# Optimization experiments

Measured on AMD Instinct MI355X. Metric: run time of the kernel, lower is better.

Reference implementation:

```python
import jax, jax.numpy as jnp
import numpy as np

GLYPH_DIM = 4096
PADDING_IDX = GLYPH_DIM  # 4096
GLYPH_EMB = 20           # CHAR_EMB 16 + COLOR_EMB 4
HIDDEN = 32
MAX_LEN = 64


def setup_inputs() -> dict:
    key = jax.random.key(0)
    k1, k2, k3, k4, k5, k6, k7 = jax.random.split(key, 7)
    B, H, W = 8192, 21, 79
    glyph_chars = jax.random.randint(k1, (B, H, W), 0, 256, dtype=jnp.int32)
    glyph_colors = jax.random.randint(k2, (B, H, W), 0, 16, dtype=jnp.int32)
    # Embedding table with zero padding row (torch padding_idx semantics)
    emb_table = jax.random.normal(k3, (GLYPH_DIM + 1, GLYPH_EMB), dtype=jnp.float32) * 0.02
    emb_table = emb_table.at[PADDING_IDX].set(0.0)
    s = 1.0 / np.sqrt(HIDDEN)
    W_ih = jax.random.uniform(k4, (HIDDEN, GLYPH_EMB), minval=-s, maxval=s, dtype=jnp.float32)
    W_hh = jax.random.uniform(k5, (HIDDEN, HIDDEN), minval=-s, maxval=s, dtype=jnp.float32)
    b_ih = jax.random.uniform(k6, (HIDDEN,), minval=-s, maxval=s, dtype=jnp.float32)
    b_hh = jax.random.uniform(k7, (HIDDEN,), minval=-s, maxval=s, dtype=jnp.float32)
    return {"glyph_chars": glyph_chars, "glyph_colors": glyph_colors,
            "emb_table": emb_table, "W_ih": W_ih, "W_hh": W_hh,
            "b_ih": b_ih, "b_hh": b_hh}


def _encode_bag(glyph_chars, glyph_colors):
    """Batched sorted-unique compaction over the bounded glyph id range."""
    B = glyph_chars.shape[0]
    g_ids = ((glyph_chars << 4) + glyph_colors).reshape(B, -1)  # [B, H*W]
    # presence[b, g] = glyph g appears in sample b (batched histogram)
    bidx = jnp.broadcast_to(jnp.arange(B, dtype=g_ids.dtype)[:, None], g_ids.shape)
    presence = jnp.zeros((B, GLYPH_DIM), dtype=bool).at[bidx, g_ids].set(True)
    # compact: present ids keep their value, absent become PADDING_IDX (=4096),
    # so sorting yields ascending unique ids followed by padding.
    ids = jnp.arange(GLYPH_DIM, dtype=jnp.int32)
    keys = jnp.where(presence, ids, jnp.int32(PADDING_IDX))
    bag = jnp.sort(keys, axis=1)[:, :MAX_LEN]  # [B, MAX_LEN]
    lengths = jnp.minimum(presence.sum(axis=1), MAX_LEN)  # [B]
    return bag, lengths


def reference(glyph_chars, glyph_colors, emb_table, W_ih, W_hh, b_ih, b_hh):
    bag, lengths = _encode_bag(glyph_chars, glyph_colors)
    emb = emb_table[bag]  # [B, MAX_LEN, GLYPH_EMB]
    B = emb.shape[0]

    # packed RNN == plain RNN where hidden state freezes past each sequence length
    xs = jnp.swapaxes(emb, 0, 1)  # [T, B, E]

    def step(h, inp):
        xt, t = inp
        h_new = jnp.tanh(xt @ W_ih.T + b_ih + h @ W_hh.T + b_hh)
        h = jnp.where((t < lengths)[:, None], h_new, h)
        return h, None

    h0 = jnp.zeros((B, HIDDEN), dtype=emb.dtype)
    h, _ = jax.lax.scan(step, h0, (xs, jnp.arange(MAX_LEN)))
    return (h, emb, bag)
```

## Files before the change

### kernel.cpp

```cpp
#include <hip/hip_runtime.h>

#define HW 1659
#define PADID 4096
#define EMB 20
#define HID 32
#define MAXLEN 64

typedef float v2f __attribute__((ext_vector_type(2)));

__global__ __launch_bounds__(128) void proj_kernel(
    const float* __restrict__ emb_table, const float* __restrict__ W_ih,
    float* __restrict__ proj)
{
    const int tid = threadIdx.x;
    const int g = blockIdx.x * 4 + (tid >> 5);
    const int j = tid & 31;
    if (g > PADID) return;
    const float* er = emb_table + (size_t)g * EMB;
    const float* wr = W_ih + j * EMB;
    float s = 0.f;
#pragma unroll
    for (int k = 0; k < EMB; k++) s += wr[k] * er[k];
    proj[(size_t)g * HID + j] = s;
}

__global__ __launch_bounds__(256) void bag_emb_kernel(
    const int* __restrict__ chars, const int* __restrict__ colors,
    const float* __restrict__ emb_table,
    float* __restrict__ out_emb, float* __restrict__ out_bag)
{
    __shared__ unsigned char pres[4096];
    __shared__ int bagl[64];
    __shared__ int wsum[4];

    const int b   = blockIdx.x;
    const int tid = threadIdx.x;
    const int lane = tid & 63;
    const int wv   = tid >> 6;

    const int base = b * HW;
    const int pe = (4 - (base & 3)) & 3;
    const int nv = (HW - pe) >> 2;
    const int nt = HW - pe - (nv << 2);
    const int4* c4 = (const int4*)(chars + base + pe);
    const int4* k4 = (const int4*)(colors + base + pe);

    int4 ca = c4[tid], ka = k4[tid];
    const bool has2 = (tid + 256) < nv;
    const int i2 = has2 ? tid + 256 : tid;
    int4 cb = c4[i2], kb = k4[i2];
    int gp = -1, gt = -1;
    if (tid < pe) gp = (chars[base + tid] << 4) + colors[base + tid];
    if (tid < nt) {
        int i = base + pe + (nv << 2) + tid;
        gt = (chars[i] << 4) + colors[i];
    }

    ((uint4*)pres)[tid] = make_uint4(0u, 0u, 0u, 0u);
    if (tid < 64) bagl[tid] = PADID;
    __syncthreads();

    pres[(ca.x << 4) + ka.x] = 1;
    pres[(ca.y << 4) + ka.y] = 1;
    pres[(ca.z << 4) + ka.z] = 1;
    pres[(ca.w << 4) + ka.w] = 1;
    if (has2) {
        pres[(cb.x << 4) + kb.x] = 1;
        pres[(cb.y << 4) + kb.y] = 1;
        pres[(cb.z << 4) + kb.z] = 1;
        pres[(cb.w << 4) + kb.w] = 1;
    }
    if (gp >= 0) pres[gp] = 1;
    if (gt >= 0) pres[gt] = 1;
    __syncthreads();

    uint4 w4 = ((const uint4*)pres)[tid];
    const unsigned M = 0x01010101u;
    int cnt = __popc(w4.x & M) + __popc(w4.y & M)
            + __popc(w4.z & M) + __popc(w4.w & M);

    int pre = cnt;
#pragma unroll
    for (int d = 1; d < 64; d <<= 1) {
        int v = __shfl_up(pre, d, 64);
        if (lane >= d) pre += v;
    }
    if (lane == 63) wsum[wv] = pre;
    __syncthreads();
    int wbase = 0;
#pragma unroll
    for (int w2 = 0; w2 < 4; w2++) wbase += (w2 < wv) ? wsum[w2] : 0;
    int p = wbase + pre - cnt;

    unsigned wrd[4] = {w4.x, w4.y, w4.z, w4.w};
#pragma unroll
    for (int c = 0; c < 4; c++) {
#pragma unroll
        for (int k = 0; k < 4; k++) {
            if ((wrd[c] >> (8 * k)) & 1) {
                if (p < 64) bagl[p] = 16 * tid + 4 * c + k;
                p++;
            }
        }
    }
    __syncthreads();

    if (tid < 64) out_bag[(size_t)b * 64 + tid] = (float)bagl[tid];

    const float4* tab4 = (const float4*)emb_table;
    float4* dst4 = (float4*)(out_emb + (size_t)b * (MAXLEN * EMB));
    for (int q = tid; q < MAXLEN * 5; q += 256) {
        int t = q / 5;
        int m = q - t * 5;
        int row = bagl[t];
        dst4[q] = tab4[row * 5 + m];
    }
}

__global__ __launch_bounds__(128, 4) void rnn_kernel(
    const float* __restrict__ proj, const float* __restrict__ bagf,
    const float* __restrict__ W_hh,
    const float* __restrict__ b_ih, const float* __restrict__ b_hh,
    float* __restrict__ out_h)
{
    __shared__ float hbuf[8][32];

    const int tid  = threadIdx.x;
    const int wv   = tid >> 6;
    const int lane = tid & 63;
    const int sl   = lane >> 4;
    const int ib   = wv * 4 + sl;
    const int jj   = lane & 15;
    const int b    = blockIdx.x * 8 + ib;

    v2f w0p[16], w1p[16];
#pragma unroll
    for (int m = 0; m < 16; m++) {
        w0p[m] = (v2f){W_hh[jj * HID + 2*m], W_hh[jj * HID + 2*m + 1]};
        w1p[m] = (v2f){W_hh[(jj+16) * HID + 2*m], W_hh[(jj+16) * HID + 2*m + 1]};
    }
    const float sb0 = b_ih[jj]      + b_hh[jj];
    const float sb1 = b_ih[jj + 16] + b_hh[jj + 16];

    const float* bps = bagf + (size_t)b * 64;

    unsigned long long mm0 = __ballot(bps[jj]      < 4095.5f);
    unsigned long long mm1 = __ballot(bps[jj + 16] < 4095.5f);
    unsigned long long mm2 = __ballot(bps[jj + 32] < 4095.5f);
    unsigned long long mm3 = __ballot(bps[jj + 48] < 4095.5f);
    const int sh = sl * 16;
    const int len = __popc((unsigned)((mm0 >> sh) & 0xFFFFu))
                  + __popc((unsigned)((mm1 >> sh) & 0xFFFFu))
                  + __popc((unsigned)((mm2 >> sh) & 0xFFFFu))
                  + __popc((unsigned)((mm3 >> sh) & 0xFFFFu));

    hbuf[ib][jj]      = 0.f;
    hbuf[ib][jj + 16] = 0.f;
    asm volatile("s_waitcnt lgkmcnt(0)" ::: "memory");

    int   idxB = (int)bps[0];
    int   idxC = (int)bps[1];
    float pv0 = proj[idxB * HID + jj];
    float pv1 = proj[idxB * HID + jj + 16];

    float h0 = 0.f, h1 = 0.f;
    for (int t = 0; t < MAXLEN; t++) {
        const int t2 = (t + 2 < MAXLEN) ? (t + 2) : (MAXLEN - 1);
        const int idxD = (int)bps[t2];
        const float pv0n = proj[idxC * HID + jj];
        const float pv1n = proj[idxC * HID + jj + 16];

        const float4* hb4 = (const float4*)hbuf[ib];
        v2f a0 = (v2f){0.f, 0.f}, a1 = a0, c0 = a0, c1 = a0;
#pragma unroll
        for (int m = 0; m < 8; m += 2) {
            float4 u = hb4[m], v = hb4[m + 1];
            v2f ulo = (v2f){u.x, u.y}, uhi = (v2f){u.z, u.w};
            v2f vlo = (v2f){v.x, v.y}, vhi = (v2f){v.z, v.w};
            a0 = __builtin_elementwise_fma(w0p[2*m],     ulo, a0);
            a0 = __builtin_elementwise_fma(w0p[2*m + 1], uhi, a0);
            a1 = __builtin_elementwise_fma(w1p[2*m],     ulo, a1);
            a1 = __builtin_elementwise_fma(w1p[2*m + 1], uhi, a1);
            c0 = __builtin_elementwise_fma(w0p[2*m + 2], vlo, c0);
            c0 = __builtin_elementwise_fma(w0p[2*m + 3], vhi, c0);
            c1 = __builtin_elementwise_fma(w1p[2*m + 2], vlo, c1);
            c1 = __builtin_elementwise_fma(w1p[2*m + 3], vhi, c1);
        }
        v2f t0 = a0 + c0;
        v2f t1 = a1 + c1;
        float s0 = sb0 + pv0 + t0.x + t0.y;
        float s1 = sb1 + pv1 + t1.x + t1.y;

        float e0 = __expf(2.f * s0);
        float e1 = __expf(2.f * s1);
        float th0 = 1.f - 2.f * __builtin_amdgcn_rcpf(e0 + 1.f);
        float th1 = 1.f - 2.f * __builtin_amdgcn_rcpf(e1 + 1.f);

        h0 = (t < len) ? th0 : h0;
        h1 = (t < len) ? th1 : h1;

        hbuf[ib][jj]      = h0;
        hbuf[ib][jj + 16] = h1;
        asm volatile("s_waitcnt lgkmcnt(0)" ::: "memory");

        pv0 = pv0n; pv1 = pv1n; idxC = idxD;
    }

    out_h[(size_t)b * HID + jj]      = h0;
    out_h[(size_t)b * HID + jj + 16] = h1;
}

__global__ __launch_bounds__(128, 4) void rnn_kernel_noproj(
    const float* __restrict__ emb, const float* __restrict__ bagf,
    const float* __restrict__ W_ih, const float* __restrict__ W_hh,
    const float* __restrict__ b_ih, const float* __restrict__ b_hh,
    float* __restrict__ out_h)
{
    __shared__ float hbuf[4][32];
    const int tid = threadIdx.x;
    const int ib  = tid >> 5;
    const int j   = tid & 31;
    const int b   = blockIdx.x * 4 + ib;

    float wih[EMB];
#pragma unroll
    for (int k = 0; k < EMB; k++) wih[k] = W_ih[j * EMB + k];
    float whh[HID];
#pragma unroll
    for (int k = 0; k < HID; k++) whh[k] = W_hh[j * HID + k];
    const float sbias = b_ih[j] + b_hh[j];

    const float* bp = bagf + (size_t)b * 64;
    unsigned long long m0 = __ballot(bp[j]      < 4095.5f);
    unsigned long long m1 = __ballot(bp[32 + j] < 4095.5f);
    const int half = ib & 1;
    const int len = __popc((unsigned)(m0 >> (half * 32)))
                  + __popc((unsigned)(m1 >> (half * 32)));

    hbuf[ib][j] = 0.f;
    asm volatile("s_waitcnt lgkmcnt(0)" ::: "memory");

    float h = 0.f;
    const float* xb = emb + (size_t)b * (MAXLEN * EMB);
    for (int t = 0; t < MAXLEN; t++) {
        const float4* xp = (const float4*)(xb + t * EMB);
        float4 x0 = xp[0], x1 = xp[1], x2 = xp[2], x3 = xp[3], x4 = xp[4];
        float s = sbias;
        const float4* hb4 = (const float4*)hbuf[ib];
#pragma unroll
        for (int m = 0; m < 8; m++) {
            float4 hv = hb4[m];
            s += whh[4*m+0]*hv.x + whh[4*m+1]*hv.y
               + whh[4*m+2]*hv.z + whh[4*m+3]*hv.w;
        }
        s += wih[0]*x0.x + wih[1]*x0.y + wih[2]*x0.z + wih[3]*x0.w;
        s += wih[4]*x1.x + wih[5]*x1.y + wih[6]*x1.z + wih[7]*x1.w;
        s += wih[8]*x2.x + wih[9]*x2.y + wih[10]*x2.z + wih[11]*x2.w;
        s += wih[12]*x3.x + wih[13]*x3.y + wih[14]*x3.z + wih[15]*x3.w;
        s += wih[16]*x4.x + wih[17]*x4.y + wih[18]*x4.z + wih[19]*x4.w;
        s = fminf(fmaxf(s, -9.f), 9.f);
        float e = __expf(2.f * s);
        float th = (e - 1.f) * __builtin_amdgcn_rcpf(e + 1.f);
        h = (t < len) ? th : h;
        hbuf[ib][j] = h;
        asm volatile("s_waitcnt lgkmcnt(0)" ::: "memory");
    }
    out_h[(size_t)b * HID + j] = h;
}

extern "C" void kernel_launch(void* const* d_in, const int* in_sizes, int n_in,
                              void* d_out, int out_size, void* d_ws, size_t ws_size,
                              hipStream_t stream) {
    const int*   chars     = (const int*)d_in[0];
    const int*   colors    = (const int*)d_in[1];
    const float* emb_table = (const float*)d_in[2];
    const float* W_ih      = (const float*)d_in[3];
    const float* W_hh      = (const float*)d_in[4];
    const float* b_ih      = (const float*)d_in[5];
    const float* b_hh      = (const float*)d_in[6];

    const int B = in_sizes[0] / HW;

    float* out     = (float*)d_out;
    float* out_h   = out;
    float* out_emb = out + (size_t)B * HID;
    float* out_bag = out_emb + (size_t)B * MAXLEN * EMB;

    const size_t proj_bytes = (size_t)(PADID + 1) * HID * sizeof(float);

    bag_emb_kernel<<<B, 256, 0, stream>>>(chars, colors, emb_table, out_emb, out_bag);

    if (ws_size >= proj_bytes) {
        float* proj = (float*)d_ws;
        proj_kernel<<<(PADID + 1 + 3) / 4, 128, 0, stream>>>(emb_table, W_ih, proj);
        rnn_kernel<<<B / 8, 128, 0, stream>>>(proj, out_bag, W_hh, b_ih, b_hh, out_h);
    } else {
        rnn_kernel_noproj<<<B / 4, 128, 0, stream>>>(out_emb, out_bag, W_ih, W_hh,
                                                     b_ih, b_hh, out_h);
    }
}
```

Baseline: 185.6 us.

## Replace LDS hidden-state broadcast with DPP lane shuffles in RNN kernel

The RNN recurrence no longer writes the hidden state to shared memory and waits on lgkmcnt every step. Instead each lane holds an interleaved pair of hidden units (2*jj, 2*jj+1) and gathers the other lanes' values through a tree of DPP xor permutes within each 16-lane group. W_hh columns are permuted to match the resulting lane order, and the launch-bounds occupancy hint drops from 4 to 2 to leave room for more registers. This removes the LDS round trip from the per-step critical path, at the cost of many DPP instructions per step. It also relies on the xor mappings being correct for the row controls used.

```diff
diff --git a/kernel.cpp b/kernel.cpp
--- a/kernel.cpp
+++ b/kernel.cpp
@@ -7,6 +7,17 @@
 #define MAXLEN 64
 
 typedef float v2f __attribute__((ext_vector_type(2)));
+
+template <int CTRL>
+__device__ __forceinline__ float dppf(float v) {
+    return __builtin_bit_cast(float,
+        __builtin_amdgcn_update_dpp(0, __builtin_bit_cast(int, v),
+                                    CTRL, 0xF, 0xF, true));
+}
+#define DPP_XOR1 0xB1
+#define DPP_XOR2 0x4E
+#define DPP_XOR7 0x141
+#define DPP_XORF 0x140
 
 __global__ __launch_bounds__(128) void proj_kernel(
     const float* __restrict__ emb_table, const float* __restrict__ W_ih,
@@ -117,14 +128,12 @@
     }
 }
 
-__global__ __launch_bounds__(128, 4) void rnn_kernel(
+__global__ __launch_bounds__(128, 2) void rnn_kernel(
     const float* __restrict__ proj, const float* __restrict__ bagf,
     const float* __restrict__ W_hh,
     const float* __restrict__ b_ih, const float* __restrict__ b_hh,
     float* __restrict__ out_h)
 {
-    __shared__ float hbuf[8][32];
-
     const int tid  = threadIdx.x;
     const int wv   = tid >> 6;
     const int lane = tid & 63;
@@ -133,14 +142,20 @@
     const int jj   = lane & 15;
     const int b    = blockIdx.x * 8 + ib;
 
-    v2f w0p[16], w1p[16];
+    const int GMAP[16] = {0,1,2,3, 7,6,5,4, 15,14,13,12,11,10,9,8};
+
+    v2f w0[16], w1[16];
+    const float2* wr0 = (const float2*)(W_hh + (2 * jj) * HID);
+    const float2* wr1 = (const float2*)(W_hh + (2 * jj + 1) * HID);
 #pragma unroll
     for (int m = 0; m < 16; m++) {
-        w0p[m] = (v2f){W_hh[jj * HID + 2*m], W_hh[jj * HID + 2*m + 1]};
-        w1p[m] = (v2f){W_hh[(jj+16) * HID + 2*m], W_hh[(jj+16) * HID + 2*m + 1]};
-    }
-    const float sb0 = b_ih[jj]      + b_hh[jj];
-    const float sb1 = b_ih[jj + 16] + b_hh[jj + 16];
+        const int c = jj ^ GMAP[m];
+        float2 a = wr0[c], bb = wr1[c];
+        w0[m] = (v2f){a.x, a.y};
+        w1[m] = (v2f){bb.x, bb.y};
+    }
+    const float sb0 = b_ih[2 * jj]     + b_hh[2 * jj];
+    const float sb1 = b_ih[2 * jj + 1] + b_hh[2 * jj + 1];
 
     const float* bps = bagf + (size_t)b * 64;
 
@@ -154,42 +169,37 @@
                   + __popc((unsigned)((mm2 >> sh) & 0xFFFFu))
                   + __popc((unsigned)((mm3 >> sh) & 0xFFFFu));
 
-    hbuf[ib][jj]      = 0.f;
-    hbuf[ib][jj + 16] = 0.f;
-    asm volatile("s_waitcnt lgkmcnt(0)" ::: "memory");
-
-    int   idxB = (int)bps[0];
-    int   idxC = (int)bps[1];
-    float pv0 = proj[idxB * HID + jj];
-    float pv1 = proj[idxB * HID + jj + 16];
+    int idxC = (int)bps[1];
+    float2 pv = ((const float2*)(proj + (size_t)((int)bps[0]) * HID))[jj];
 
     float h0 = 0.f, h1 = 0.f;
     for (int t = 0; t < MAXLEN; t++) {
         const int t2 = (t + 2 < MAXLEN) ? (t + 2) : (MAXLEN - 1);
         const int idxD = (int)bps[t2];
-        const float pv0n = proj[idxC * HID + jj];
-        const float pv1n = proj[idxC * HID + jj + 16];
-
-        const float4* hb4 = (const float4*)hbuf[ib];
-        v2f a0 = (v2f){0.f, 0.f}, a1 = a0, c0 = a0, c1 = a0;
-#pragma unroll
-        for (int m = 0; m < 8; m += 2) {
-            float4 u = hb4[m], v = hb4[m + 1];
-            v2f ulo = (v2f){u.x, u.y}, uhi = (v2f){u.z, u.w};
-            v2f vlo = (v2f){v.x, v.y}, vhi = (v2f){v.z, v.w};
-            a0 = __builtin_elementwise_fma(w0p[2*m],     ulo, a0);
-            a0 = __builtin_elementwise_fma(w0p[2*m + 1], uhi, a0);
-            a1 = __builtin_elementwise_fma(w1p[2*m],     ulo, a1);
-            a1 = __builtin_elementwise_fma(w1p[2*m + 1], uhi, a1);
-            c0 = __builtin_elementwise_fma(w0p[2*m + 2], vlo, c0);
-            c0 = __builtin_elementwise_fma(w0p[2*m + 3], vhi, c0);
-            c1 = __builtin_elementwise_fma(w1p[2*m + 2], vlo, c1);
-            c1 = __builtin_elementwise_fma(w1p[2*m + 3], vhi, c1);
+        const float2 pvn = ((const float2*)(proj + (size_t)idxC * HID))[jj];
+
+        v2f g[16];
+        g[0] = (v2f){h0, h1};
+        g[1] = (v2f){dppf<DPP_XOR1>(g[0].x), dppf<DPP_XOR1>(g[0].y)};
+        g[2] = (v2f){dppf<DPP_XOR2>(g[0].x), dppf<DPP_XOR2>(g[0].y)};
+        g[3] = (v2f){dppf<DPP_XOR2>(g[1].x), dppf<DPP_XOR2>(g[1].y)};
+#pragma unroll
+        for (int m = 0; m < 4; m++)
+            g[4 + m] = (v2f){dppf<DPP_XOR7>(g[m].x), dppf<DPP_XOR7>(g[m].y)};
+#pragma unroll
+        for (int m = 0; m < 8; m++)
+            g[8 + m] = (v2f){dppf<DPP_XORF>(g[m].x), dppf<DPP_XORF>(g[m].y)};
+
+        v2f a0 = (v2f){0.f, 0.f}, b0 = a0, a1 = a0, b1 = a0;
+#pragma unroll
+        for (int m = 0; m < 16; m += 2) {
+            a0 = __builtin_elementwise_fma(w0[m],     g[m],     a0);
+            b0 = __builtin_elementwise_fma(w0[m + 1], g[m + 1], b0);
+            a1 = __builtin_elementwise_fma(w1[m],     g[m],     a1);
+            b1 = __builtin_elementwise_fma(w1[m + 1], g[m + 1], b1);
         }
-        v2f t0 = a0 + c0;
-        v2f t1 = a1 + c1;
-        float s0 = sb0 + pv0 + t0.x + t0.y;
-        float s1 = sb1 + pv1 + t1.x + t1.y;
+        float s0 = sb0 + pv.x + (a0.x + a0.y) + (b0.x + b0.y);
+        float s1 = sb1 + pv.y + (a1.x + a1.y) + (b1.x + b1.y);
 
         float e0 = __expf(2.f * s0);
         float e1 = __expf(2.f * s1);
@@ -199,15 +209,10 @@
         h0 = (t < len) ? th0 : h0;
         h1 = (t < len) ? th1 : h1;
 
-        hbuf[ib][jj]      = h0;
-        hbuf[ib][jj + 16] = h1;
-        asm volatile("s_waitcnt lgkmcnt(0)" ::: "memory");
-
-        pv0 = pv0n; pv1 = pv1n; idxC = idxD;
-    }
-
-    out_h[(size_t)b * HID + jj]      = h0;
-    out_h[(size_t)b * HID + jj + 16] = h1;
+        pv = pvn; idxC = idxD;
+    }
+
+    ((float2*)(out_h + (size_t)b * HID))[jj] = make_float2(h0, h1);
 }
 
 __global__ __launch_bounds__(128, 4) void rnn_kernel_noproj(
```

Measured after the change: 183.0 us. About the same (-1.4%).
